# Optimization experiments

Hardware: AMD Instinct MI355X
Metric: run time of the kernel (lower is better)

## Reference

```python
import jax, jax.numpy as jnp
import numpy as np

NEG_INF = -1e30


def setup_inputs() -> dict:
    key = jax.random.key(0)
    ks = jax.random.split(key, 11)
    b, n, d = 4, 2048, 1024
    scale = 1.0 / np.sqrt(d)
    inp = {
        "q": jax.random.normal(ks[0], (b, n, d), jnp.float32),
        "k": jax.random.normal(ks[1], (b, n, d), jnp.float32),
        "v": jax.random.normal(ks[2], (b, n, d), jnp.float32),
        # nn.Linear params: weight [out, in], bias [out]
        "Wq": jax.random.normal(ks[3], (d, d), jnp.float32) * scale,
        "bq": jnp.zeros((d,), jnp.float32),
        "Wk": jax.random.normal(ks[4], (d, d), jnp.float32) * scale,
        "bk": jnp.zeros((d,), jnp.float32),
        "Wv": jax.random.normal(ks[5], (d, d), jnp.float32) * scale,
        "bv": jnp.zeros((d,), jnp.float32),
        "Wo": jax.random.normal(ks[6], (d, d), jnp.float32) * scale,
        "bo": jnp.zeros((d,), jnp.float32),
    }
    return inp


def reference(q, k, v, Wq, bq, Wk, bk, Wv, bv, Wo, bo):
    # Faithful to source: the multi-head reshape/transpose results are never
    # assigned, so attention runs single-headed over full n_embd vectors.
    b, n, d = q.shape
    qp = q @ Wq.T + bq  # [b, n, d]
    kp = k @ Wk.T + bk
    vp = v @ Wv.T + bv
    scale = jnp.asarray(1.0 / d, qp.dtype) ** 0.5  # sqrt(1/d)
    att = jnp.einsum('bnd,bmd->bnm', qp, kp) * scale  # [b, n, n]
    causal = jnp.tril(jnp.ones((n, n), bool))          # block_size tril sliced to n
    att = jnp.where(causal[None, :, :], att, NEG_INF)
    att = jax.nn.softmax(att, axis=-1)  # dropout p=0.0 -> identity
    y = att @ vp                        # [b, n, d]
    # source bug reproduced: transpose(1,2) then reshape(b, n, d)
    y = jnp.swapaxes(y, 1, 2).reshape(b, n, d)
    y = y @ Wo.T + bo
    return y
```

## Files before the change

kernel.cpp:

```cpp
#include <hip/hip_runtime.h>
#include <hip/hip_bf16.h>
#include <stdint.h>

typedef __bf16 bf16_t;
typedef __bf16 bf16x8 __attribute__((ext_vector_type(8)));
typedef __bf16 bf16x4 __attribute__((ext_vector_type(4)));
typedef float f32x4 __attribute__((ext_vector_type(4)));

#define GLD_LDS16(src, dst)                                                              \
  __builtin_amdgcn_global_load_lds((const __attribute__((address_space(1))) void*)(src), \
                                   (__attribute__((address_space(3))) void*)(dst), 16, 0, 0)

struct CvtArgs {
  const float* src[7];
  bf16_t* dst[7];
  long n4[7];
};

__global__ __launch_bounds__(256) void cvt_all(CvtArgs a) {
  const int seg = blockIdx.y;
  const float* __restrict__ in = a.src[seg];
  bf16_t* __restrict__ out = a.dst[seg];
  const long n4 = a.n4[seg];
  long i = (long)blockIdx.x * blockDim.x + threadIdx.x;
  const long stride = (long)gridDim.x * blockDim.x;
  for (; i < n4; i += stride) {
    float4 v = ((const float4*)in)[i];
    bf16x4 o;
    o[0] = (bf16_t)v.x; o[1] = (bf16_t)v.y; o[2] = (bf16_t)v.z; o[3] = (bf16_t)v.w;
    ((bf16x4*)out)[i] = o;
  }
}

__global__ __launch_bounds__(256) void softmax_causal(bf16_t* __restrict__ S, int n, long sB) {
  const int i = blockIdx.x;
  const int z = blockIdx.y;
  bf16_t* row = S + (long)z * sB + (long)i * n;
  const int t = threadIdx.x;
  const int j0 = t << 3;
  const int jmax = ((i >> 7) + 1) << 7;
  const bool active = j0 < jmax;

  float vals[8];
  float mx = -3.0e38f;
  if (active) {
    bf16x8 vv = ((const bf16x8*)row)[t];
#pragma unroll
    for (int e = 0; e < 8; ++e) {
      float v = (j0 + e <= i) ? (float)vv[e] : -3.0e38f;
      vals[e] = v;
      mx = fmaxf(mx, v);
    }
  }
#pragma unroll
  for (int off = 32; off; off >>= 1) mx = fmaxf(mx, __shfl_xor(mx, off));
  __shared__ float redm[4];
  if ((t & 63) == 0) redm[t >> 6] = mx;
  __syncthreads();
  mx = fmaxf(fmaxf(redm[0], redm[1]), fmaxf(redm[2], redm[3]));

  float sum = 0.f;
  if (active) {
#pragma unroll
    for (int e = 0; e < 8; ++e) {
      float p = (j0 + e <= i) ? __expf(vals[e] - mx) : 0.f;
      vals[e] = p;
      sum += p;
    }
  }
#pragma unroll
  for (int off = 32; off; off >>= 1) sum += __shfl_xor(sum, off);
  __shared__ float reds[4];
  if ((t & 63) == 0) reds[t >> 6] = sum;
  __syncthreads();
  sum = reds[0] + reds[1] + reds[2] + reds[3];
  const float inv = 1.0f / sum;

  if (active) {
    bf16x8 o;
#pragma unroll
    for (int e = 0; e < 8; ++e) o[e] = (bf16_t)(vals[e] * inv);
    ((bf16x8*)row)[t] = o;
  }
}

__device__ __forceinline__ void xcd_remap(int& bx, int& by, int& bz) {
  const int gx = gridDim.x, gy = gridDim.y;
  int lin = (blockIdx.z * gy + blockIdx.y) * gx + blockIdx.x;
  const int nwg = gx * gy * (int)gridDim.z;
  lin = (lin & 7) * (nwg >> 3) + (lin >> 3);
  bx = lin % gx;
  const int rem = lin / gx;
  by = rem % gy;
  bz = rem / gy;
}

template <int EPI, bool BIAS, bool KBOUND>
__device__ __forceinline__ void gemm_body(const bf16_t* __restrict__ A,
                                          const bf16_t* __restrict__ B,
                                          const float* __restrict__ bias,
                                          void* __restrict__ Cout,
                                          int N, int K, float alpha,
                                          int m0, int n0) {
  int KT = K >> 5;
  if (KBOUND) {
    int kb = (n0 + 128) >> 5;
    if (kb < KT) KT = kb;
  }

  __shared__ __align__(16) bf16_t As[128 * 32];
  __shared__ __align__(16) bf16_t Bs[128 * 32];

  const int t = threadIdx.x;
  const int l = t & 63;
  const int w = t >> 6;
  const int wr = w >> 1, wc = w & 1;

  const int c0 = t, c1 = t + 256;
  const bf16_t* a_src0 = A + (long)(m0 + (c0 >> 2)) * K + ((c0 & 3) << 3);
  const bf16_t* a_src1 = A + (long)(m0 + (c1 >> 2)) * K + ((c1 & 3) << 3);
  const bf16_t* b_src0 = B + (long)(n0 + (c0 >> 2)) * K + ((c0 & 3) << 3);
  const bf16_t* b_src1 = B + (long)(n0 + (c1 >> 2)) * K + ((c1 & 3) << 3);
  char* const asb = (char*)As;
  char* const bsb = (char*)Bs;
  char* const a_dst0 = asb + w * 1024;
  char* const a_dst1 = asb + 4096 + w * 1024;
  char* const b_dst0 = bsb + w * 1024;
  char* const b_dst1 = bsb + 4096 + w * 1024;

  const int r16 = l & 15, kg = l >> 4;
  int aoff[4], boff[4];
#pragma unroll
  for (int mi = 0; mi < 4; ++mi) aoff[mi] = (((wr * 64 + mi * 16 + r16) * 32) + kg * 8) * 2;
#pragma unroll
  for (int ni = 0; ni < 4; ++ni) boff[ni] = (((wc * 64 + ni * 16 + r16) * 32) + kg * 8) * 2;

  f32x4 acc[4][4] = {};

  for (int kt = 0; kt < KT; ++kt) {
    __syncthreads();
    GLD_LDS16(a_src0, a_dst0);
    GLD_LDS16(a_src1, a_dst1);
    GLD_LDS16(b_src0, b_dst0);
    GLD_LDS16(b_src1, b_dst1);
    a_src0 += 32; a_src1 += 32; b_src0 += 32; b_src1 += 32;
    __syncthreads();

    bf16x8 af[4], bfr[4];
#pragma unroll
    for (int mi = 0; mi < 4; ++mi) af[mi] = *(const bf16x8*)(asb + aoff[mi]);
#pragma unroll
    for (int ni = 0; ni < 4; ++ni) bfr[ni] = *(const bf16x8*)(bsb + boff[ni]);
#pragma unroll
    for (int mi = 0; mi < 4; ++mi)
#pragma unroll
      for (int ni = 0; ni < 4; ++ni)
        acc[mi][ni] = __builtin_amdgcn_mfma_f32_16x16x32_bf16(af[mi], bfr[ni], acc[mi][ni], 0, 0, 0);
  }

  const int rowbase = m0 + wr * 64 + ((l >> 4) << 2);
  const int colbase = n0 + wc * 64 + (l & 15);
  if constexpr (EPI == 0) {
    float* C = (float*)Cout;
#pragma unroll
    for (int mi = 0; mi < 4; ++mi)
#pragma unroll
      for (int ni = 0; ni < 4; ++ni) {
        const int col = colbase + ni * 16;
        float badd = 0.f;
        if constexpr (BIAS) badd = bias[col];
#pragma unroll
        for (int j = 0; j < 4; ++j)
          C[(long)(rowbase + mi * 16 + j) * N + col] = acc[mi][ni][j] * alpha + badd;
      }
  } else if constexpr (EPI == 1) {
    bf16_t* C = (bf16_t*)Cout;
#pragma unroll
    for (int mi = 0; mi < 4; ++mi)
#pragma unroll
      for (int ni = 0; ni < 4; ++ni) {
        const int col = colbase + ni * 16;
        float badd = 0.f;
        if constexpr (BIAS) badd = bias[col];
#pragma unroll
        for (int j = 0; j < 4; ++j)
          C[(long)(rowbase + mi * 16 + j) * N + col] = (bf16_t)(acc[mi][ni][j] * alpha + badd);
      }
  } else {
    bf16_t* C = (bf16_t*)Cout;
#pragma unroll
    for (int mi = 0; mi < 4; ++mi)
#pragma unroll
      for (int ni = 0; ni < 4; ++ni) {
        const int col = colbase + ni * 16;
        float badd = 0.f;
        if constexpr (BIAS) badd = bias[col];
        const int row0 = rowbase + mi * 16;
        const int batch = row0 >> 11, nr = row0 & 2047;
        bf16x4 o;
#pragma unroll
        for (int j = 0; j < 4; ++j) o[j] = (bf16_t)(acc[mi][ni][j] + badd);
        *(bf16x4*)(C + (long)batch * (2048 * 1024) + (long)col * 2048 + nr) = o;
      }
  }
}

template <int EPI, bool BIAS, bool KBOUND>
__global__ __launch_bounds__(256, 4) void gemm_bt(const bf16_t* __restrict__ Ag,
                                                  const bf16_t* __restrict__ Bg,
                                                  const float* __restrict__ bias,
                                                  void* __restrict__ Cout,
                                                  int N, int K, float alpha,
                                                  long sAb, long sBb, long sCb, int eltC) {
  int bx, by, bz;
  xcd_remap(bx, by, bz);
  const int m0 = by << 7, n0 = bx << 7;
  gemm_body<EPI, BIAS, KBOUND>(Ag + (long)bz * sAb, Bg + (long)bz * sBb, bias,
                               (char*)Cout + (long)bz * sCb * eltC, N, K, alpha, m0, n0);
}

struct QkArgs {
  const bf16_t* A[2];
  const bf16_t* W[2];
  const float* bias[2];
  bf16_t* C[2];
};

__global__ __launch_bounds__(256, 4) void gemm_qk(QkArgs a, int N, int K) {
  int bx, by, bz;
  xcd_remap(bx, by, bz);
  gemm_body<1, true, false>(a.A[bz], a.W[bz], a.bias[bz], a.C[bz], N, K, 1.0f,
                            by << 7, bx << 7);
}

struct FsvArgs {
  const bf16_t* qp;
  const bf16_t* kp;
  bf16_t* S;
  const bf16_t* vB;
  const bf16_t* Wv;
  const float* bv;
  bf16_t* vpT;
  long nd, nn;
};

__global__ __launch_bounds__(256, 4) void fused_sv(FsvArgs a) {
  int bx, by, bz;
  xcd_remap(bx, by, bz);
  if (bz < 4) {
    const int m0 = by << 7, n0 = bx << 7;
    if (n0 > m0 + 127) return;
    gemm_body<1, false, false>(a.qp + (long)bz * a.nd, a.kp + (long)bz * a.nd, nullptr,
                               a.S + (long)bz * a.nn, 2048, 1024, 0.03125f, m0, n0);
  } else {
    const int lin = (bz - 4) * 256 + by * 16 + bx;
    const int m0 = (lin >> 3) << 7, n0 = (lin & 7) << 7;
    gemm_body<2, true, false>(a.vB, a.Wv, a.bv, a.vpT, 1024, 1024, 1.0f, m0, n0);
  }
}

extern "C" void kernel_launch(void* const* d_in, const int* in_sizes, int n_in,
                              void* d_out, int out_size, void* d_ws, size_t ws_size,
                              hipStream_t stream) {
  const int b = 4, n = 2048, d = 1024;
  const long nd  = (long)n * d;
  const long bn  = (long)b * n;
  const long bnd = bn * d;
  const long ddl = (long)d * d;
  const long nn  = (long)n * n;

  const float* q  = (const float*)d_in[0];
  const float* k  = (const float*)d_in[1];
  const float* v  = (const float*)d_in[2];
  const float* Wq = (const float*)d_in[3];
  const float* bq = (const float*)d_in[4];
  const float* Wk = (const float*)d_in[5];
  const float* bk = (const float*)d_in[6];
  const float* Wv = (const float*)d_in[7];
  const float* bv = (const float*)d_in[8];
  const float* Wo = (const float*)d_in[9];
  const float* bo = (const float*)d_in[10];

  bf16_t* ws  = (bf16_t*)d_ws;
  bf16_t* qB  = ws;
  bf16_t* kB  = qB + bnd;
  bf16_t* vB  = kB + bnd;
  bf16_t* WqB = vB + bnd;
  bf16_t* WkB = WqB + ddl;
  bf16_t* WvB = WkB + ddl;
  bf16_t* WoB = WvB + ddl;
  bf16_t* qpB = WoB + ddl;
  bf16_t* kpB = qpB + bnd;
  bf16_t* vpT = kpB + bnd;
  bf16_t* S   = vpT + bnd;
  bf16_t* yT  = S + (long)b * nn;
  const size_t need = (size_t)(7 * bnd + 4 * ddl + (long)b * nn) * 2;
  if (ws_size < need) return;

  dim3 blk(256);

  CvtArgs ca;
  ca.src[0] = q;  ca.dst[0] = qB;  ca.n4[0] = bnd / 4;
  ca.src[1] = k;  ca.dst[1] = kB;  ca.n4[1] = bnd / 4;
  ca.src[2] = v;  ca.dst[2] = vB;  ca.n4[2] = bnd / 4;
  ca.src[3] = Wq; ca.dst[3] = WqB; ca.n4[3] = ddl / 4;
  ca.src[4] = Wk; ca.dst[4] = WkB; ca.n4[4] = ddl / 4;
  ca.src[5] = Wv; ca.dst[5] = WvB; ca.n4[5] = ddl / 4;
  ca.src[6] = Wo; ca.dst[6] = WoB; ca.n4[6] = ddl / 4;
  cvt_all<<<dim3(512, 7), blk, 0, stream>>>(ca);

  QkArgs qa;
  qa.A[0] = qB; qa.W[0] = WqB; qa.bias[0] = bq; qa.C[0] = qpB;
  qa.A[1] = kB; qa.W[1] = WkB; qa.bias[1] = bk; qa.C[1] = kpB;
  gemm_qk<<<dim3(d / 128, bn / 128, 2), blk, 0, stream>>>(qa, d, d);

  FsvArgs fa;
  fa.qp = qpB; fa.kp = kpB; fa.S = S;
  fa.vB = vB; fa.Wv = WvB; fa.bv = bv; fa.vpT = vpT;
  fa.nd = nd; fa.nn = nn;
  fused_sv<<<dim3(16, 16, 6), blk, 0, stream>>>(fa);

  softmax_causal<<<dim3(n, b), blk, 0, stream>>>(S, n, nn);

  gemm_bt<1, false, true><<<dim3(n / 128, d / 128, b), blk, 0, stream>>>(
      vpT, S, nullptr, yT, n, n, 1.f, nd, nn, nd, 2);

  gemm_bt<0, true, false><<<dim3(d / 128, bn / 128, 1), blk, 0, stream>>>(
      yT, WoB, bo, (float*)d_out, d, d, 1.f, 0, 0, 0, 4);
}
```

Baseline: 218.5 us.

## Double GEMM K-tile with XOR-swizzled LDS and regroup QKV/score launches

The shared GEMM core now stages a K tile of 64 instead of 32, using a 32KB LDS buffer with an XOR swizzle on 16-byte chunks to avoid bank conflicts, and halves the number of sync/load iterations. The Q/K/V projections are merged into one three-way launch, and the V projection's transposed output goes through an LDS transpose so global stores are coalesced 16-byte writes. The causal score GEMM becomes a separate gemm_bt launch with early exit for upper-triangle tiles. Occupancy bound drops from 4 to 3 blocks per SM because of the larger LDS footprint.

```diff
diff --git a/kernel.cpp b/kernel.cpp
--- a/kernel.cpp
+++ b/kernel.cpp
@@ -95,118 +95,71 @@
   bz = rem / gy;
 }
 
-template <int EPI, bool BIAS, bool KBOUND>
-__device__ __forceinline__ void gemm_body(const bf16_t* __restrict__ A,
+__device__ __forceinline__ void gemm_core(char* smem,
+                                          const bf16_t* __restrict__ A,
                                           const bf16_t* __restrict__ B,
-                                          const float* __restrict__ bias,
-                                          void* __restrict__ Cout,
-                                          int N, int K, float alpha,
-                                          int m0, int n0) {
-  int KT = K >> 5;
-  if (KBOUND) {
-    int kb = (n0 + 128) >> 5;
-    if (kb < KT) KT = kb;
-  }
-
-  __shared__ __align__(16) bf16_t As[128 * 32];
-  __shared__ __align__(16) bf16_t Bs[128 * 32];
-
+                                          int K, int KT, int m0, int n0,
+                                          f32x4 (&acc)[4][4]) {
+  char* const asb = smem;
+  char* const bsb = smem + 16384;
   const int t = threadIdx.x;
   const int l = t & 63;
   const int w = t >> 6;
   const int wr = w >> 1, wc = w & 1;
-
-  const int c0 = t, c1 = t + 256;
-  const bf16_t* a_src0 = A + (long)(m0 + (c0 >> 2)) * K + ((c0 & 3) << 3);
-  const bf16_t* a_src1 = A + (long)(m0 + (c1 >> 2)) * K + ((c1 & 3) << 3);
-  const bf16_t* b_src0 = B + (long)(n0 + (c0 >> 2)) * K + ((c0 & 3) << 3);
-  const bf16_t* b_src1 = B + (long)(n0 + (c1 >> 2)) * K + ((c1 & 3) << 3);
-  char* const asb = (char*)As;
-  char* const bsb = (char*)Bs;
-  char* const a_dst0 = asb + w * 1024;
-  char* const a_dst1 = asb + 4096 + w * 1024;
-  char* const b_dst0 = bsb + w * 1024;
-  char* const b_dst1 = bsb + 4096 + w * 1024;
-
   const int r16 = l & 15, kg = l >> 4;
-  int aoff[4], boff[4];
-#pragma unroll
-  for (int mi = 0; mi < 4; ++mi) aoff[mi] = (((wr * 64 + mi * 16 + r16) * 32) + kg * 8) * 2;
-#pragma unroll
-  for (int ni = 0; ni < 4; ++ni) boff[ni] = (((wc * 64 + ni * 16 + r16) * 32) + kg * 8) * 2;
-
-  f32x4 acc[4][4] = {};
+
+  const bf16_t* a_src[4];
+  const bf16_t* b_src[4];
+#pragma unroll
+  for (int i = 0; i < 4; ++i) {
+    const int c = i * 256 + t;
+    const int row = c >> 3;
+    const int sl = (c & 7) ^ (row & 7);
+    a_src[i] = A + (long)(m0 + row) * K + sl * 8;
+    b_src[i] = B + (long)(n0 + row) * K + sl * 8;
+  }
+
+  int aoff[2][4], boff[2][4];
+#pragma unroll
+  for (int kp = 0; kp < 2; ++kp)
+#pragma unroll
+    for (int mi = 0; mi < 4; ++mi) {
+      const int ra = wr * 64 + mi * 16 + r16;
+      aoff[kp][mi] = ra * 128 + ((kp * 4 + kg) ^ (ra & 7)) * 16;
+      const int rb = wc * 64 + mi * 16 + r16;
+      boff[kp][mi] = rb * 128 + ((kp * 4 + kg) ^ (rb & 7)) * 16;
+    }
 
   for (int kt = 0; kt < KT; ++kt) {
     __syncthreads();
-    GLD_LDS16(a_src0, a_dst0);
-    GLD_LDS16(a_src1, a_dst1);
-    GLD_LDS16(b_src0, b_dst0);
-    GLD_LDS16(b_src1, b_dst1);
-    a_src0 += 32; a_src1 += 32; b_src0 += 32; b_src1 += 32;
+#pragma unroll
+    for (int i = 0; i < 4; ++i) {
+      GLD_LDS16(a_src[i], asb + i * 4096 + w * 1024);
+      GLD_LDS16(b_src[i], bsb + i * 4096 + w * 1024);
+      a_src[i] += 64;
+      b_src[i] += 64;
+    }
     __syncthreads();
 
-    bf16x8 af[4], bfr[4];
-#pragma unroll
-    for (int mi = 0; mi < 4; ++mi) af[mi] = *(const bf16x8*)(asb + aoff[mi]);
-#pragma unroll
-    for (int ni = 0; ni < 4; ++ni) bfr[ni] = *(const bf16x8*)(bsb + boff[ni]);
-#pragma unroll
-    for (int mi = 0; mi < 4; ++mi)
-#pragma unroll
-      for (int ni = 0; ni < 4; ++ni)
-        acc[mi][ni] = __builtin_amdgcn_mfma_f32_16x16x32_bf16(af[mi], bfr[ni], acc[mi][ni], 0, 0, 0);
-  }
-
-  const int rowbase = m0 + wr * 64 + ((l >> 4) << 2);
-  const int colbase = n0 + wc * 64 + (l & 15);
-  if constexpr (EPI == 0) {
-    float* C = (float*)Cout;
-#pragma unroll
-    for (int mi = 0; mi < 4; ++mi)
-#pragma unroll
-      for (int ni = 0; ni < 4; ++ni) {
-        const int col = colbase + ni * 16;
-        float badd = 0.f;
-        if constexpr (BIAS) badd = bias[col];
-#pragma unroll
-        for (int j = 0; j < 4; ++j)
-          C[(long)(rowbase + mi * 16 + j) * N + col] = acc[mi][ni][j] * alpha + badd;
-      }
-  } else if constexpr (EPI == 1) {
-    bf16_t* C = (bf16_t*)Cout;
-#pragma unroll
-    for (int mi = 0; mi < 4; ++mi)
-#pragma unroll
-      for (int ni = 0; ni < 4; ++ni) {
-        const int col = colbase + ni * 16;
-        float badd = 0.f;
-        if constexpr (BIAS) badd = bias[col];
-#pragma unroll
-        for (int j = 0; j < 4; ++j)
-          C[(long)(rowbase + mi * 16 + j) * N + col] = (bf16_t)(acc[mi][ni][j] * alpha + badd);
-      }
-  } else {
-    bf16_t* C = (bf16_t*)Cout;
-#pragma unroll
-    for (int mi = 0; mi < 4; ++mi)
-#pragma unroll
-      for (int ni = 0; ni < 4; ++ni) {
-        const int col = colbase + ni * 16;
-        float badd = 0.f;
-        if constexpr (BIAS) badd = bias[col];
-        const int row0 = rowbase + mi * 16;
-        const int batch = row0 >> 11, nr = row0 & 2047;
-        bf16x4 o;
-#pragma unroll
-        for (int j = 0; j < 4; ++j) o[j] = (bf16_t)(acc[mi][ni][j] + badd);
-        *(bf16x4*)(C + (long)batch * (2048 * 1024) + (long)col * 2048 + nr) = o;
-      }
-  }
-}
-
-template <int EPI, bool BIAS, bool KBOUND>
-__global__ __launch_bounds__(256, 4) void gemm_bt(const bf16_t* __restrict__ Ag,
+#pragma unroll
+    for (int kp = 0; kp < 2; ++kp) {
+      bf16x8 af[4], bfr[4];
+#pragma unroll
+      for (int mi = 0; mi < 4; ++mi) af[mi] = *(const bf16x8*)(asb + aoff[kp][mi]);
+#pragma unroll
+      for (int ni = 0; ni < 4; ++ni) bfr[ni] = *(const bf16x8*)(bsb + boff[kp][ni]);
+#pragma unroll
+      for (int mi = 0; mi < 4; ++mi)
+#pragma unroll
+        for (int ni = 0; ni < 4; ++ni)
+          acc[mi][ni] =
+              __builtin_amdgcn_mfma_f32_16x16x32_bf16(af[mi], bfr[ni], acc[mi][ni], 0, 0, 0);
+    }
+  }
+}
+
+template <int EPI, bool BIAS, bool CAUSAL, bool KBOUND>
+__global__ __launch_bounds__(256, 3) void gemm_bt(const bf16_t* __restrict__ Ag,
                                                   const bf16_t* __restrict__ Bg,
                                                   const float* __restrict__ bias,
                                                   void* __restrict__ Cout,
@@ -215,47 +168,115 @@
   int bx, by, bz;
   xcd_remap(bx, by, bz);
   const int m0 = by << 7, n0 = bx << 7;
-  gemm_body<EPI, BIAS, KBOUND>(Ag + (long)bz * sAb, Bg + (long)bz * sBb, bias,
-                               (char*)Cout + (long)bz * sCb * eltC, N, K, alpha, m0, n0);
-}
-
-struct QkArgs {
-  const bf16_t* A[2];
-  const bf16_t* W[2];
-  const float* bias[2];
-  bf16_t* C[2];
+  if (CAUSAL && n0 > m0 + 127) return;
+
+  int KT = K >> 6;
+  if (KBOUND) {
+    const int kb = (n0 + 128) >> 6;
+    if (kb < KT) KT = kb;
+  }
+
+  __shared__ __align__(16) char smem[32768];
+  f32x4 acc[4][4] = {};
+  gemm_core(smem, Ag + (long)bz * sAb, Bg + (long)bz * sBb, K, KT, m0, n0, acc);
+
+  const int t = threadIdx.x;
+  const int l = t & 63;
+  const int w = t >> 6;
+  const int wr = w >> 1, wc = w & 1;
+  const int rowbase = m0 + wr * 64 + ((l >> 4) << 2);
+  const int colbase = n0 + wc * 64 + (l & 15);
+  if constexpr (EPI == 0) {
+    float* C = (float*)((char*)Cout + (long)bz * sCb * eltC);
+#pragma unroll
+    for (int mi = 0; mi < 4; ++mi)
+#pragma unroll
+      for (int ni = 0; ni < 4; ++ni) {
+        const int col = colbase + ni * 16;
+        float badd = 0.f;
+        if constexpr (BIAS) badd = bias[col];
+#pragma unroll
+        for (int j = 0; j < 4; ++j)
+          C[(long)(rowbase + mi * 16 + j) * N + col] = acc[mi][ni][j] * alpha + badd;
+      }
+  } else {
+    bf16_t* C = (bf16_t*)((char*)Cout + (long)bz * sCb * eltC);
+#pragma unroll
+    for (int mi = 0; mi < 4; ++mi)
+#pragma unroll
+      for (int ni = 0; ni < 4; ++ni) {
+        const int col = colbase + ni * 16;
+        float badd = 0.f;
+        if constexpr (BIAS) badd = bias[col];
+#pragma unroll
+        for (int j = 0; j < 4; ++j)
+          C[(long)(rowbase + mi * 16 + j) * N + col] = (bf16_t)(acc[mi][ni][j] * alpha + badd);
+      }
+  }
+}
+
+struct Qkv3Args {
+  const bf16_t* A[3];
+  const bf16_t* W[3];
+  const float* bias[3];
+  bf16_t* C[3];
 };
 
-__global__ __launch_bounds__(256, 4) void gemm_qk(QkArgs a, int N, int K) {
+__global__ __launch_bounds__(256, 3) void qkv3(Qkv3Args ga, int N, int K) {
   int bx, by, bz;
   xcd_remap(bx, by, bz);
-  gemm_body<1, true, false>(a.A[bz], a.W[bz], a.bias[bz], a.C[bz], N, K, 1.0f,
-                            by << 7, bx << 7);
-}
-
-struct FsvArgs {
-  const bf16_t* qp;
-  const bf16_t* kp;
-  bf16_t* S;
-  const bf16_t* vB;
-  const bf16_t* Wv;
-  const float* bv;
-  bf16_t* vpT;
-  long nd, nn;
-};
-
-__global__ __launch_bounds__(256, 4) void fused_sv(FsvArgs a) {
-  int bx, by, bz;
-  xcd_remap(bx, by, bz);
-  if (bz < 4) {
-    const int m0 = by << 7, n0 = bx << 7;
-    if (n0 > m0 + 127) return;
-    gemm_body<1, false, false>(a.qp + (long)bz * a.nd, a.kp + (long)bz * a.nd, nullptr,
-                               a.S + (long)bz * a.nn, 2048, 1024, 0.03125f, m0, n0);
+  const int m0 = by << 7, n0 = bx << 7;
+
+  __shared__ __align__(16) char smem[32768];
+  f32x4 acc[4][4] = {};
+  gemm_core(smem, ga.A[bz], ga.W[bz], K, K >> 6, m0, n0, acc);
+
+  const float* __restrict__ bias = ga.bias[bz];
+  const int t = threadIdx.x;
+  const int l = t & 63;
+  const int w = t >> 6;
+  const int wr = w >> 1, wc = w & 1;
+  const int r16 = l & 15, kg = l >> 4;
+
+  if (bz < 2) {
+    bf16_t* C = ga.C[bz];
+    const int rowbase = m0 + wr * 64 + kg * 4;
+    const int colbase = n0 + wc * 64 + r16;
+#pragma unroll
+    for (int mi = 0; mi < 4; ++mi)
+#pragma unroll
+      for (int ni = 0; ni < 4; ++ni) {
+        const int col = colbase + ni * 16;
+        const float badd = bias[col];
+#pragma unroll
+        for (int j = 0; j < 4; ++j)
+          C[(long)(rowbase + mi * 16 + j) * N + col] = (bf16_t)(acc[mi][ni][j] + badd);
+      }
   } else {
-    const int lin = (bz - 4) * 256 + by * 16 + bx;
-    const int m0 = (lin >> 3) << 7, n0 = (lin & 7) << 7;
-    gemm_body<2, true, false>(a.vB, a.Wv, a.bv, a.vpT, 1024, 1024, 1.0f, m0, n0);
+    __syncthreads();
+    bf16_t* tt = (bf16_t*)smem;
+#pragma unroll
+    for (int mi = 0; mi < 4; ++mi)
+#pragma unroll
+      for (int ni = 0; ni < 4; ++ni) {
+        const int lc = wc * 64 + ni * 16 + r16;
+        const int lr = wr * 64 + mi * 16 + kg * 4;
+        const float badd = bias[n0 + lc];
+        bf16x4 o;
+#pragma unroll
+        for (int j = 0; j < 4; ++j) o[j] = (bf16_t)(acc[mi][ni][j] + badd);
+        *(bf16x4*)(tt + lc * 128 + lr) = o;
+      }
+    __syncthreads();
+    bf16_t* C = ga.C[2];
+    const int batch = m0 >> 11, nb = m0 & 2047;
+#pragma unroll
+    for (int i = 0; i < 8; ++i) {
+      const int c = i * 256 + t;
+      const int lc = c >> 4, ch = c & 15;
+      *(bf16x8*)(C + (long)batch * (2048 * 1024) + (long)(n0 + lc) * 2048 + nb + ch * 8) =
+          *(const bf16x8*)(tt + lc * 128 + ch * 8);
+    }
   }
 }
 
@@ -309,22 +330,20 @@
   ca.src[6] = Wo; ca.dst[6] = WoB; ca.n4[6] = ddl / 4;
   cvt_all<<<dim3(512, 7), blk, 0, stream>>>(ca);
 
-  QkArgs qa;
+  Qkv3Args qa;
   qa.A[0] = qB; qa.W[0] = WqB; qa.bias[0] = bq; qa.C[0] = qpB;
   qa.A[1] = kB; qa.W[1] = WkB; qa.bias[1] = bk; qa.C[1] = kpB;
-  gemm_qk<<<dim3(d / 128, bn / 128, 2), blk, 0, stream>>>(qa, d, d);
-
-  FsvArgs fa;
-  fa.qp = qpB; fa.kp = kpB; fa.S = S;
-  fa.vB = vB; fa.Wv = WvB; fa.bv = bv; fa.vpT = vpT;
-  fa.nd = nd; fa.nn = nn;
-  fused_sv<<<dim3(16, 16, 6), blk, 0, stream>>>(fa);
+  qa.A[2] = vB; qa.W[2] = WvB; qa.bias[2] = bv; qa.C[2] = vpT;
+  qkv3<<<dim3(d / 128, bn / 128, 3), blk, 0, stream>>>(qa, d, d);
+
+  gemm_bt<1, false, true, false><<<dim3(n / 128, n / 128, b), blk, 0, stream>>>(
+      qpB, kpB, nullptr, S, n, d, 0.03125f, nd, nd, nn, 2);
 
   softmax_causal<<<dim3(n, b), blk, 0, stream>>>(S, n, nn);
 
-  gemm_bt<1, false, true><<<dim3(n / 128, d / 128, b), blk, 0, stream>>>(
+  gemm_bt<1, false, false, true><<<dim3(n / 128, d / 128, b), blk, 0, stream>>>(
       vpT, S, nullptr, yT, n, n, 1.f, nd, nn, nd, 2);
 
-  gemm_bt<0, true, false><<<dim3(d / 128, bn / 128, 1), blk, 0, stream>>>(
+  gemm_bt<0, true, false, false><<<dim3(d / 128, bn / 128, 1), blk, 0, stream>>>(
       yT, WoB, bo, (float*)d_out, d, d, 1.f, 0, 0, 0, 4);
 }
```

Result: faster. 187.6 us (-14.1%).
